# Kernel tuning notes

Measured on AMD Instinct MI355X. Metric: run time of the kernel, lower is better.

Reference implementation:

```python
import jax, jax.numpy as jnp
import numpy as np

D, H, K = 384, 6, 8

def _ln(x, g, b, eps=1e-5):
    mu = jnp.mean(x, axis=-1, keepdims=True)
    var = jnp.mean((x - mu) ** 2, axis=-1, keepdims=True)
    return (x - mu) * jax.lax.rsqrt(var + eps) * g + b

def setup_inputs() -> dict:
    key = jax.random.key(0)
    ks = jax.random.split(key, 20)
    B, N = 4, 2048
    s = 0.02
    inp = {
        'x': jax.random.normal(ks[0], (B, N, D), jnp.float32),
        'knn_index': jax.random.randint(ks[1], (B * K * N,), 0, B * N, jnp.int64),
        'ln1_g': jnp.ones((D,), jnp.float32),
        'ln1_b': jnp.zeros((D,), jnp.float32),
        'w_qkv': jax.random.normal(ks[2], (D, 3 * D), jnp.float32) * s,
        'w_proj': jax.random.normal(ks[3], (D, D), jnp.float32) * s,
        'b_proj': jnp.zeros((D,), jnp.float32),
        'w_knn': jax.random.normal(ks[4], (2 * D, D), jnp.float32) * s,
        'b_knn': jnp.zeros((D,), jnp.float32),
        'w_g1': jax.random.normal(ks[5], (2 * D, D), jnp.float32) * s,
        'b_g1': jnp.zeros((D,), jnp.float32),
        'w_g2': jax.random.normal(ks[6], (D, D), jnp.float32) * s,
        'b_g2': jnp.zeros((D,), jnp.float32),
        'ln2_g': jnp.ones((D,), jnp.float32),
        'ln2_b': jnp.zeros((D,), jnp.float32),
        'w_fc1': jax.random.normal(ks[7], (D, 4 * D), jnp.float32) * s,
        'b_fc1': jnp.zeros((4 * D,), jnp.float32),
        'w_fc2': jax.random.normal(ks[8], (4 * D, D), jnp.float32) * s,
        'b_fc2': jnp.zeros((D,), jnp.float32),
    }
    return inp

def reference(x, knn_index, ln1_g, ln1_b, w_qkv, w_proj, b_proj, w_knn, b_knn,
              w_g1, b_g1, w_g2, b_g2, ln2_g, ln2_b, w_fc1, b_fc1, w_fc2, b_fc2):
    B, N, _ = x.shape
    hd = D // H
    scale = hd ** -0.5
    nx = _ln(x, ln1_g, ln1_b)
    # --- self attention ---
    qkv = (nx @ w_qkv).reshape(B, N, 3, H, hd).transpose(2, 0, 3, 1, 4)  # [3,B,H,N,hd]
    q, k, v = qkv[0], qkv[1], qkv[2]
    attn = jax.nn.softmax(jnp.einsum('bhnd,bhmd->bhnm', q * scale, k), axis=-1)
    attn_out = jnp.einsum('bhnm,bhmd->bhnd', attn, v).transpose(0, 2, 1, 3).reshape(B, N, D)
    attn_out = attn_out @ w_proj + b_proj
    # --- EdgeConv-style graph feature: gather-concat-MLP-maxpool ---
    feat = nx.reshape(B * N, D)[knn_index].reshape(B, K, N, D)
    xe = jnp.broadcast_to(nx[:, None], (B, K, N, D))
    gf = jnp.concatenate([feat - xe, xe], axis=-1)  # [B,K,N,2D]
    knn_out = jnp.max(jax.nn.leaky_relu(gf @ w_knn + b_knn, 0.2), axis=1)  # [B,N,D]
    # --- salience gate ---
    gi = jnp.concatenate([attn_out, knn_out], axis=-1)
    gate = jax.nn.sigmoid(jax.nn.gelu(gi @ w_g1 + b_g1, approximate=False) @ w_g2 + b_g2)
    fused = (1 - gate) * attn_out + gate * knn_out
    x = x + fused
    # --- FFN ---
    h = jax.nn.gelu(_ln(x, ln2_g, ln2_b) @ w_fc1 + b_fc1, approximate=False)
    x = x + (h @ w_fc2 + b_fc2)
    return x
```

## Files before the change

kernel.cpp:

```cpp
#include <hip/hip_runtime.h>
#include <math.h>

typedef unsigned short u16;
typedef __attribute__((ext_vector_type(8))) short short8;
typedef __attribute__((ext_vector_type(4))) float floatx4;
typedef __attribute__((ext_vector_type(16))) float floatx16;
typedef __attribute__((ext_vector_type(4))) short sh4v;
typedef __attribute__((ext_vector_type(2))) unsigned uint2v;

union sh4u { sh4v v; u16 u[4]; };
union sh8u { short8 v; u16 u[8]; };
union sh8w { short8 v; unsigned w[4]; };

__device__ __forceinline__ floatx4 mfma16(short8 a, short8 b, floatx4 c) {
  return __builtin_amdgcn_mfma_f32_16x16x32_bf16(a, b, c, 0, 0, 0);
}
__device__ __forceinline__ floatx16 mfma32(short8 a, short8 b, floatx16 c) {
  return __builtin_amdgcn_mfma_f32_32x32x16_bf16(a, b, c, 0, 0, 0);
}

__device__ __forceinline__ floatx4 zero4() {
  floatx4 z = {0.f, 0.f, 0.f, 0.f};
  return z;
}
__device__ __forceinline__ floatx16 zero16() {
  floatx16 z;
#pragma unroll
  for (int i = 0; i < 16; i++) z[i] = 0.f;
  return z;
}

__device__ __forceinline__ float hexp2(float x) {
  return __builtin_amdgcn_exp2f(x);
}

__device__ __forceinline__ u16 f2b(float f) {
  union { float f; unsigned u; } v; v.f = f;
  unsigned u = v.u;
  return (u16)((u + 0x7FFFu + ((u >> 16) & 1u)) >> 16);
}

__device__ __forceinline__ float b2f(u16 u) {
  union { unsigned u; float f; } v; v.u = ((unsigned)u) << 16;
  return v.f;
}

__device__ __forceinline__ float blo(unsigned w) {
  union { unsigned u; float f; } v; v.u = w << 16;
  return v.f;
}
__device__ __forceinline__ float bhi(unsigned w) {
  union { unsigned u; float f; } v; v.u = w & 0xFFFF0000u;
  return v.f;
}

__device__ __forceinline__ float gelu_exact(float x) {
  return 0.5f * x * (1.f + erff(x * 0.70710678118654752440f));
}

__device__ __forceinline__ unsigned pack2(float a, float b) {
  return (unsigned)f2b(a) | ((unsigned)f2b(b) << 16);
}

__device__ __forceinline__ unsigned permpack(float p0, float p1) {
  return __builtin_amdgcn_perm(__float_as_uint(p1), __float_as_uint(p0), 0x07060302u);
}

__global__ __launch_bounds__(256) void tcln_kernel(
    const float* __restrict__ p0, const float* __restrict__ p1,
    const float* __restrict__ p2, const float* __restrict__ p3,
    const float* __restrict__ p4, const float* __restrict__ p5,
    const float* __restrict__ wknn,
    u16* __restrict__ o0, u16* __restrict__ o1, u16* __restrict__ o2,
    u16* __restrict__ o3, u16* __restrict__ o4, u16* __restrict__ o5,
    u16* __restrict__ wcT,
    const float* __restrict__ x, const float* __restrict__ g,
    const float* __restrict__ bia, u16* __restrict__ nx) {
  __shared__ u16 L[64][66];
  int t = blockIdx.x, tid = threadIdx.x;
  if (t >= 612) {
    int wave = tid >> 6, lane = tid & 63;
    int row = (t - 612) * 4 + wave;
    const float* xr = x + (size_t)row * 384;
    float v[6];
    float s = 0.f;
#pragma unroll
    for (int j = 0; j < 6; j++) { v[j] = xr[lane + 64 * j]; s += v[j]; }
#pragma unroll
    for (int off = 32; off > 0; off >>= 1) s += __shfl_xor(s, off);
    float mu = s * (1.f / 384.f);
    float ss = 0.f;
#pragma unroll
    for (int j = 0; j < 6; j++) { float d = v[j] - mu; ss += d * d; }
#pragma unroll
    for (int off = 32; off > 0; off >>= 1) ss += __shfl_xor(ss, off);
    float rstd = rsqrtf(ss * (1.f / 384.f) + 1e-5f);
    u16* orow = nx + (size_t)row * 384;
#pragma unroll
    for (int j = 0; j < 6; j++) {
      int d = lane + 64 * j;
      orow[d] = f2b((v[j] - mu) * rstd * g[d] + bia[d]);
    }
    return;
  }
  if (t >= 540) {
    t -= 540;
    int tk = t / 12, tn = t % 12;
    int k0 = tk * 64, j0 = tn * 64;
#pragma unroll
    for (int i = 0; i < 4; i++) {
      int c = tid + 256 * i;
      int r = c >> 4, c4 = (c & 15) * 4;
      floatx4 v;
      if (j0 < 384) {
        v = *(const floatx4*)(wknn + (size_t)(k0 + r) * 384 + j0 + c4);
      } else {
        floatx4 a = *(const floatx4*)(wknn + (size_t)(384 + k0 + r) * 384 + (j0 - 384) + c4);
        floatx4 b = *(const floatx4*)(wknn + (size_t)(k0 + r) * 384 + (j0 - 384) + c4);
        v = a - b;
      }
      *(unsigned*)&L[r][c4]     = pack2(v[0], v[1]);
      *(unsigned*)&L[r][c4 + 2] = pack2(v[2], v[3]);
    }
    __syncthreads();
#pragma unroll
    for (int i = 0; i < 2; i++) {
      int c = tid + 256 * i;
      int nn = c >> 3, k8 = (c & 7) * 8;
      sh8u pk;
#pragma unroll
      for (int j = 0; j < 8; j++) pk.u[j] = L[k8 + j][nn];
      *(short8*)(wcT + (size_t)(j0 + nn) * 384 + k0 + k8) = pk.v;
    }
    return;
  }
  const float* src; u16* dst; int Kd, Nd, tk, tn;
  if      (t < 108) { src = p0; dst = o0; Kd = 384;  Nd = 1152; tk = t / 18; tn = t % 18; }
  else if (t < 144) { src = p1; dst = o1; Kd = 384;  Nd = 384;  t -= 108; tk = t / 6;  tn = t % 6; }
  else if (t < 216) { src = p2; dst = o2; Kd = 768;  Nd = 384;  t -= 144; tk = t / 6;  tn = t % 6; }
  else if (t < 252) { src = p3; dst = o3; Kd = 384;  Nd = 384;  t -= 216; tk = t / 6;  tn = t % 6; }
  else if (t < 396) { src = p4; dst = o4; Kd = 384;  Nd = 1536; t -= 252; tk = t / 24; tn = t % 24; }
  else              { src = p5; dst = o5; Kd = 1536; Nd = 384;  t -= 396; tk = t / 6;  tn = t % 6; }
  int k0 = tk * 64, n0 = tn * 64;
#pragma unroll
  for (int i = 0; i < 4; i++) {
    int c = tid + 256 * i;
    int r = c >> 4, c4 = (c & 15) * 4;
    floatx4 v = *(const floatx4*)(src + (size_t)(k0 + r) * Nd + n0 + c4);
    *(unsigned*)&L[r][c4]     = pack2(v[0], v[1]);
    *(unsigned*)&L[r][c4 + 2] = pack2(v[2], v[3]);
  }
  __syncthreads();
#pragma unroll
  for (int i = 0; i < 2; i++) {
    int c = tid + 256 * i;
    int nn = c >> 3, k8 = (c & 7) * 8;
    sh8u pk;
#pragma unroll
    for (int j = 0; j < 8; j++) pk.u[j] = L[k8 + j][nn];
    *(short8*)(dst + (size_t)(n0 + nn) * Kd + k0 + k8) = pk.v;
  }
}

__global__ __launch_bounds__(256) void lnb_kernel(const u16* __restrict__ x,
                                                  const float* __restrict__ g,
                                                  const float* __restrict__ bia,
                                                  u16* __restrict__ out) {
  int wave = threadIdx.x >> 6, lane = threadIdx.x & 63;
  int row = blockIdx.x * 4 + wave;
  const u16* xr = x + (size_t)row * 384;
  float v[6];
  float s = 0.f;
#pragma unroll
  for (int j = 0; j < 6; j++) { v[j] = b2f(xr[lane + 64 * j]); s += v[j]; }
#pragma unroll
  for (int off = 32; off > 0; off >>= 1) s += __shfl_xor(s, off);
  float mu = s * (1.f / 384.f);
  float ss = 0.f;
#pragma unroll
  for (int j = 0; j < 6; j++) { float d = v[j] - mu; ss += d * d; }
#pragma unroll
  for (int off = 32; off > 0; off >>= 1) ss += __shfl_xor(ss, off);
  float rstd = rsqrtf(ss * (1.f / 384.f) + 1e-5f);
  u16* orow = out + (size_t)row * 384;
#pragma unroll
  for (int j = 0; j < 6; j++) {
    int d = lane + 64 * j;
    orow[d] = f2b((v[j] - mu) * rstd * g[d] + bia[d]);
  }
}

template <int EPI>
__global__ __launch_bounds__(256) void gemm64_kernel(
    const u16* __restrict__ A0, const u16* __restrict__ A1, int Ksplit,
    const u16* __restrict__ BwT, const u16* __restrict__ BwT2, int N, int K,
    const float* __restrict__ bias,
    float* __restrict__ outF, u16* __restrict__ outB, u16* __restrict__ outB2,
    const u16* __restrict__ eA16, const u16* __restrict__ eK16,
    const float* __restrict__ eX, u16* __restrict__ outV) {
  __shared__ u16 As[64][72];
  __shared__ u16 Bs[128][72];
  int tid = threadIdx.x;
  int lane = tid & 63, w = tid >> 6, quad = lane >> 4, l16 = lane & 15;
  int n0 = blockIdx.x * 128, m0 = blockIdx.y * 64;
  int ra = tid >> 3, ca = (tid & 7) * 8;
  const u16* Bsrc = BwT;
  int nbase = n0;
  if (EPI == 8 && n0 >= 1152) { Bsrc = BwT2; nbase = n0 - 1152; }
  floatx4 acc[4][2];
#pragma unroll
  for (int i = 0; i < 4; i++)
#pragma unroll
    for (int j = 0; j < 2; j++) acc[i][j] = zero4();

  short8 pa[2], pb[4];
  auto loadAB = [&](int k0) {
    const u16* Ap;
    int kk, sA;
    if (k0 < Ksplit) { Ap = A0; kk = k0; sA = Ksplit; }
    else             { Ap = A1; kk = k0 - Ksplit; sA = K - Ksplit; }
    pa[0] = *(const short8*)(Ap + (size_t)(m0 + ra) * sA + kk + ca);
    pa[1] = *(const short8*)(Ap + (size_t)(m0 + ra + 32) * sA + kk + ca);
#pragma unroll
    for (int i = 0; i < 4; i++)
      pb[i] = *(const short8*)(Bsrc + (size_t)(nbase + ra + 32 * i) * K + k0 + ca);
  };
  loadAB(0);
  int iters = K >> 6;
  for (int kt = 0; kt < iters; kt++) {
    __syncthreads();
    *(short8*)&As[ra][ca] = pa[0];
    *(short8*)&As[ra + 32][ca] = pa[1];
#pragma unroll
    for (int i = 0; i < 4; i++) *(short8*)&Bs[ra + 32 * i][ca] = pb[i];
    __syncthreads();
    if (kt + 1 < iters) loadAB((kt + 1) * 64);
#pragma unroll
    for (int kh = 0; kh < 2; kh++) {
      short8 af[4], bfr[2];
#pragma unroll
      for (int mt = 0; mt < 4; mt++)
        af[mt] = *(const short8*)&As[mt * 16 + l16][kh * 32 + quad * 8];
#pragma unroll
      for (int nt = 0; nt < 2; nt++)
        bfr[nt] = *(const short8*)&Bs[w * 32 + nt * 16 + l16][kh * 32 + quad * 8];
#pragma unroll
      for (int mt = 0; mt < 4; mt++)
#pragma unroll
        for (int nt = 0; nt < 2; nt++)
          acc[mt][nt] = mfma16(af[mt], bfr[nt], acc[mt][nt]);
    }
  }

#pragma unroll
  for (int mt = 0; mt < 4; mt++)
#pragma unroll
    for (int nt = 0; nt < 2; nt++) {
      int col = n0 + w * 32 + nt * 16 + l16;
      int row0 = m0 + mt * 16 + quad * 4;
      if (EPI == 8) {
        if (col < 1152) {
          float sc = (col < 384) ? 0.18033688011112042f : 1.f;
          sh4u pk;
#pragma unroll
          for (int r = 0; r < 4; r++) {
            u16 bv = f2b(acc[mt][nt][r] * sc);
            outB[(size_t)(row0 + r) * 1152 + col] = bv;
            pk.u[r] = bv;
          }
          if (col >= 768) {
            int b = row0 >> 11, n = row0 & 2047;
            int hd = col - 768;
            *(sh4v*)(outV + ((size_t)(b * 6 + (hd >> 6)) * 64 + (hd & 63)) * 2048 + n) = pk.v;
          }
        } else {
#pragma unroll
          for (int r = 0; r < 4; r++)
            outB2[(size_t)(row0 + r) * 768 + (col - 1152)] = f2b(acc[mt][nt][r]);
        }
      } else {
#pragma unroll
        for (int r = 0; r < 4; r++) {
          size_t rc = (size_t)(row0 + r) * N + col;
          float v = acc[mt][nt][r];
          if (EPI == 3) {
            outB[rc] = f2b(gelu_exact(v + bias[col]));
          } else if (EPI == 4) {
            float gte = 1.f / (1.f + hexp2(-1.44269504088896f * (v + bias[col])));
            float fu = (1.f - gte) * b2f(eA16[rc]) + gte * b2f(eK16[rc]);
            outB[rc] = f2b(eX[rc] + fu);
          } else if (EPI == 7) {
            outF[rc] = v + bias[col] + b2f(eA16[rc]);
          }
        }
      }
    }
}

__global__ __launch_bounds__(256) void attnknn_kernel(
    const u16* __restrict__ qkv, const u16* __restrict__ Vt,
    u16* __restrict__ OPb, float* __restrict__ LS,
    const u16* __restrict__ GBb, const int* __restrict__ kidx,
    const float* __restrict__ bknn, u16* __restrict__ knn_bf) {
  __shared__ u16 Ks[2][64][72];
  __shared__ u16 Vts[2][64][72];
  int bid = blockIdx.x, tid = threadIdx.x;
  int lane = tid & 63, w = tid >> 6;
  if (bid >= 1536) {
    int row = (bid - 1536) * 4 + w;
    int b = row >> 11, n = row & 2047;
    const unsigned* browp = (const unsigned*)(GBb + (size_t)row * 768 + 384);
    uint2v bw01 = *(const uint2v*)(browp + 2 * lane);
    unsigned bw2 = browp[128 + lane];
    floatx4 bk4 = *(const floatx4*)(bknn + 4 * lane);
    float bk40 = bknn[256 + 2 * lane], bk41 = bknn[256 + 2 * lane + 1];
    int gi[8];
#pragma unroll
    for (int kk = 0; kk < 8; kk++) gi[kk] = kidx[(b * 8 + kk) * 2048 + n];
    float mx[6];
#pragma unroll
    for (int e = 0; e < 6; e++) mx[e] = -1e30f;
#pragma unroll
    for (int kk = 0; kk < 8; kk++) {
      const unsigned* gp = (const unsigned*)(GBb + (size_t)gi[kk] * 768);
      uint2v g01 = *(const uint2v*)(gp + 2 * lane);
      unsigned g2 = gp[128 + lane];
      mx[0] = fmaxf(mx[0], blo(g01[0]));
      mx[1] = fmaxf(mx[1], bhi(g01[0]));
      mx[2] = fmaxf(mx[2], blo(g01[1]));
      mx[3] = fmaxf(mx[3], bhi(g01[1]));
      mx[4] = fmaxf(mx[4], blo(g2));
      mx[5] = fmaxf(mx[5], bhi(g2));
    }
    float vv[6];
    vv[0] = mx[0] + blo(bw01[0]) + bk4[0];
    vv[1] = mx[1] + bhi(bw01[0]) + bk4[1];
    vv[2] = mx[2] + blo(bw01[1]) + bk4[2];
    vv[3] = mx[3] + bhi(bw01[1]) + bk4[3];
    vv[4] = mx[4] + blo(bw2) + bk40;
    vv[5] = mx[5] + bhi(bw2) + bk41;
#pragma unroll
    for (int e = 0; e < 6; e++) vv[e] = fmaxf(vv[e], 0.2f * vv[e]);
    unsigned* op = (unsigned*)(knn_bf + (size_t)row * 384);
    uint2v ow;
    ow[0] = pack2(vv[0], vv[1]);
    ow[1] = pack2(vv[2], vv[3]);
    *(uint2v*)(op + 2 * lane) = ow;
    op[128 + lane] = pack2(vv[4], vv[5]);
    return;
  }
  int vb = (bid & 7) * 192 + (bid >> 3);
  int split = vb / 384;
  int rr = vb - split * 384;
  int bh = rr >> 4, b = bh / 6, h = bh % 6;
  int q0 = (rr & 15) * 128;
  int ql = lane & 31, h5 = lane >> 5;
  const u16* qbase = qkv + (size_t)b * 2048 * 1152 + h * 64;
  const u16* kbase = qbase + 384 + (size_t)split * 512 * 1152;
  const u16* vtb = Vt + (size_t)bh * 64 * 2048 + split * 512;
  int qrow = q0 + w * 32 + ql;
  short8 qB[4];
#pragma unroll
  for (int s = 0; s < 4; s++)
    qB[s] = *(const short8*)(qbase + (size_t)qrow * 1152 + s * 16 + h5 * 8);
  floatx16 O[2];
  O[0] = zero16(); O[1] = zero16();
  float accLs = 0.f;

  int rb = tid >> 3, c8 = (tid & 7) * 8;
  short8 rk[2], rv[2];
  rk[0] = *(const short8*)(kbase + (size_t)rb * 1152 + c8);
  rk[1] = *(const short8*)(kbase + (size_t)(rb + 32) * 1152 + c8);
  rv[0] = *(const short8*)(vtb + (size_t)rb * 2048 + c8);
  rv[1] = *(const short8*)(vtb + (size_t)(rb + 32) * 2048 + c8);

  int cur = 0;
  for (int kt = 0; kt < 8; kt++) {
    *(short8*)&Ks[cur][rb][c8] = rk[0];
    *(short8*)&Ks[cur][rb + 32][c8] = rk[1];
    *(short8*)&Vts[cur][rb][c8] = rv[0];
    *(short8*)&Vts[cur][rb + 32][c8] = rv[1];
    __syncthreads();
    if (kt < 7) {
      int key0 = (kt + 1) * 64;
      rk[0] = *(const short8*)(kbase + (size_t)(key0 + rb) * 1152 + c8);
      rk[1] = *(const short8*)(kbase + (size_t)(key0 + rb + 32) * 1152 + c8);
      rv[0] = *(const short8*)(vtb + (size_t)rb * 2048 + key0 + c8);
      rv[1] = *(const short8*)(vtb + (size_t)(rb + 32) * 2048 + key0 + c8);
    }
#pragma unroll
    for (int t = 0; t < 2; t++) {
      floatx16 st = zero16();
#pragma unroll
      for (int s = 0; s < 4; s++) {
        short8 aK = *(const short8*)&Ks[cur][32 * t + ql][16 * s + 8 * h5];
        st = mfma32(aK, qB[s], st);
      }
      unsigned W[8];
#pragma unroll
      for (int j = 0; j < 8; j++) {
        float e0 = hexp2(st[2 * j]), e1 = hexp2(st[2 * j + 1]);
        accLs += e0 + e1;
        W[j] = permpack(e0, e1);
      }
#pragma unroll
      for (int c = 0; c < 2; c++) {
        int kk = 2 * t + c;
        uint2v s0 = __builtin_amdgcn_permlane32_swap(W[4 * c], W[4 * c + 2], false, false);
        uint2v s1 = __builtin_amdgcn_permlane32_swap(W[4 * c + 1], W[4 * c + 3], false, false);
        sh8w pb_;
        pb_.w[0] = s0[0];
        pb_.w[1] = s1[0];
        pb_.w[2] = s0[1];
        pb_.w[3] = s1[1];
        short8 aV0 = *(const short8*)&Vts[cur][ql][16 * kk + 8 * h5];
        short8 aV1 = *(const short8*)&Vts[cur][32 + ql][16 * kk + 8 * h5];
        O[0] = mfma32(aV0, pb_.v, O[0]);
        O[1] = mfma32(aV1, pb_.v, O[1]);
      }
    }
    cur ^= 1;
  }
  u16* orow = OPb + (size_t)split * 8192 * 384 + (size_t)(b * 2048 + qrow) * 384 + h * 64;
#pragma unroll
  for (int d = 0; d < 2; d++)
#pragma unroll
    for (int rq = 0; rq < 4; rq++) {
      sh4u pk;
#pragma unroll
      for (int r3 = 0; r3 < 4; r3++) pk.u[r3] = f2b(O[d][4 * rq + r3]);
      *(sh4v*)(orow + 32 * d + 8 * rq + 4 * h5) = pk.v;
    }
  uint2v sw = __builtin_amdgcn_permlane32_swap(__float_as_uint(accLs), __float_as_uint(accLs),
                                               false, false);
  if (lane < 32) LS[split * 8192 + b * 2048 + qrow] = accLs + __uint_as_float(sw[1]);
}

__global__ __launch_bounds__(256) void projc_kernel(
    const u16* __restrict__ OPb, const float* __restrict__ LS,
    const u16* __restrict__ BwT, const float* __restrict__ bias,
    u16* __restrict__ outB) {
  __shared__ u16 As[64][72];
  __shared__ u16 Bs[128][72];
  int tid = threadIdx.x;
  int lane = tid & 63, w = tid >> 6, quad = lane >> 4, l16 = lane & 15;
  int n0 = blockIdx.x * 128, m0 = blockIdx.y * 64;
  int ra = tid >> 3, ca = (tid & 7) * 8;
  const size_t SP = (size_t)8192 * 384;
  floatx4 acc[4][2];
#pragma unroll
  for (int i = 0; i < 4; i++)
#pragma unroll
    for (int j = 0; j < 2; j++) acc[i][j] = zero4();

  short8 pa[2], pb[4];
  auto loadAB = [&](int k0) {
#pragma unroll
    for (int i = 0; i < 2; i++) {
      const u16* p = OPb + (size_t)(m0 + ra + 32 * i) * 384 + k0 + ca;
      sh8u a0, a1, a2, a3, pk;
      a0.v = *(const short8*)p;
      a1.v = *(const short8*)(p + SP);
      a2.v = *(const short8*)(p + 2 * SP);
      a3.v = *(const short8*)(p + 3 * SP);
#pragma unroll
      for (int j = 0; j < 8; j++)
        pk.u[j] = f2b((b2f(a0.u[j]) + b2f(a1.u[j])) + (b2f(a2.u[j]) + b2f(a3.u[j])));
      pa[i] = pk.v;
    }
#pragma unroll
    for (int i = 0; i < 4; i++)
      pb[i] = *(const short8*)(BwT + (size_t)(n0 + ra + 32 * i) * 384 + k0 + ca);
  };
  loadAB(0);
  for (int kt = 0; kt < 6; kt++) {
    __syncthreads();
    *(short8*)&As[ra][ca] = pa[0];
    *(short8*)&As[ra + 32][ca] = pa[1];
#pragma unroll
    for (int i = 0; i < 4; i++) *(short8*)&Bs[ra + 32 * i][ca] = pb[i];
    __syncthreads();
    if (kt < 5) loadAB((kt + 1) * 64);
#pragma unroll
    for (int kh = 0; kh < 2; kh++) {
      short8 af[4], bfr[2];
#pragma unroll
      for (int mt = 0; mt < 4; mt++)
        af[mt] = *(const short8*)&As[mt * 16 + l16][kh * 32 + quad * 8];
#pragma unroll
      for (int nt = 0; nt < 2; nt++)
        bfr[nt] = *(const short8*)&Bs[w * 32 + nt * 16 + l16][kh * 32 + quad * 8];
#pragma unroll
      for (int mt = 0; mt < 4; mt++)
#pragma unroll
        for (int nt = 0; nt < 2; nt++)
          acc[mt][nt] = mfma16(af[mt], bfr[nt], acc[mt][nt]);
    }
  }
#pragma unroll
  for (int mt = 0; mt < 4; mt++) {
    int row0 = m0 + mt * 16 + quad * 4;
    float rl[4];
#pragma unroll
    for (int r = 0; r < 4; r++) {
      int gr = row0 + r;
      rl[r] = 1.f / ((LS[gr] + LS[8192 + gr]) + (LS[16384 + gr] + LS[24576 + gr]));
    }
#pragma unroll
    for (int nt = 0; nt < 2; nt++) {
      int col = n0 + w * 32 + nt * 16 + l16;
#pragma unroll
      for (int r = 0; r < 4; r++)
        outB[(size_t)(row0 + r) * 384 + col] = f2b(acc[mt][nt][r] * rl[r] + bias[col]);
    }
  }
}

extern "C" void kernel_launch(void* const* d_in, const int* in_sizes, int n_in,
                              void* d_out, int out_size, void* d_ws, size_t ws_size,
                              hipStream_t stream) {
  const float* x    = (const float*)d_in[0];
  const int* kidx   = (const int*)d_in[1];
  const float* ln1g = (const float*)d_in[2];
  const float* ln1b = (const float*)d_in[3];
  const float* wqkv = (const float*)d_in[4];
  const float* wproj= (const float*)d_in[5];
  const float* bproj= (const float*)d_in[6];
  const float* wknn = (const float*)d_in[7];
  const float* bknn = (const float*)d_in[8];
  const float* wg1  = (const float*)d_in[9];
  const float* bg1  = (const float*)d_in[10];
  const float* wg2  = (const float*)d_in[11];
  const float* bg2  = (const float*)d_in[12];
  const float* ln2g = (const float*)d_in[13];
  const float* ln2b = (const float*)d_in[14];
  const float* wfc1 = (const float*)d_in[15];
  const float* bfc1 = (const float*)d_in[16];
  const float* wfc2 = (const float*)d_in[17];
  const float* bfc2 = (const float*)d_in[18];
  float* out = (float*)d_out;

  const int M = 8192;
  char* ws = (char*)d_ws;
  size_t off = 0;
  auto alloc = [&](size_t bytes) -> char* {
    char* p = ws + off;
    off += (bytes + 255) & ~(size_t)255;
    return p;
  };
  u16* nx_bf    = (u16*)alloc((size_t)M * 384 * 2);
  u16* qkv_bf   = (u16*)alloc((size_t)M * 1152 * 2);
  u16* attn_bf  = (u16*)alloc((size_t)M * 384 * 2);
  u16* GBb      = (u16*)alloc((size_t)M * 768 * 2);
  u16* knn_bf   = (u16*)alloc((size_t)M * 384 * 2);
  u16* x2b      = (u16*)alloc((size_t)M * 384 * 2);
  u16* t1_bf    = (u16*)alloc((size_t)M * 384 * 2);
  u16* nx2_bf   = (u16*)alloc((size_t)M * 384 * 2);
  u16* Vt_b     = (u16*)alloc((size_t)24 * 64 * 2048 * 2);
  u16* OPb      = (u16*)alloc((size_t)4 * M * 384 * 2);
  float* LS     = (float*)alloc((size_t)4 * M * 4);
  u16* wqkvT    = (u16*)alloc((size_t)1152 * 384 * 2);
  u16* wprojT   = (u16*)alloc(384 * 384 * 2);
  u16* wcT      = (u16*)alloc((size_t)768 * 384 * 2);
  u16* wg1T     = (u16*)alloc((size_t)384 * 768 * 2);
  u16* wg2T     = (u16*)alloc(384 * 384 * 2);
  u16* wfc1T    = (u16*)alloc((size_t)1536 * 384 * 2);
  u16* wfc2T    = (u16*)alloc((size_t)384 * 1536 * 2);
  u16* h_bf     = qkv_bf;

  tcln_kernel<<<2660, 256, 0, stream>>>(wqkv, wproj, wg1, wg2, wfc1, wfc2, wknn,
                                        wqkvT, wprojT, wg1T, wg2T, wfc1T, wfc2T, wcT,
                                        x, ln1g, ln1b, nx_bf);
  gemm64_kernel<8><<<dim3(15, 128), 256, 0, stream>>>(nx_bf, nx_bf, 384, wqkvT, wcT, 1920, 384,
                                                      nullptr, nullptr, qkv_bf, GBb,
                                                      nullptr, nullptr, nullptr, Vt_b);
  attnknn_kernel<<<3584, 256, 0, stream>>>(qkv_bf, Vt_b, OPb, LS,
                                           GBb, kidx, bknn, knn_bf);
  projc_kernel<<<dim3(3, 128), 256, 0, stream>>>(OPb, LS, wprojT, bproj, attn_bf);
  gemm64_kernel<3><<<dim3(3, 128), 256, 0, stream>>>(attn_bf, knn_bf, 384, wg1T, nullptr, 384, 768,
                                                     bg1, nullptr, t1_bf, nullptr,
                                                     nullptr, nullptr, nullptr, nullptr);
  gemm64_kernel<4><<<dim3(3, 128), 256, 0, stream>>>(t1_bf, t1_bf, 384, wg2T, nullptr, 384, 384,
                                                     bg2, nullptr, x2b, nullptr,
                                                     attn_bf, knn_bf, x, nullptr);
  lnb_kernel<<<2048, 256, 0, stream>>>(x2b, ln2g, ln2b, nx2_bf);
  gemm64_kernel<3><<<dim3(12, 128), 256, 0, stream>>>(nx2_bf, nx2_bf, 384, wfc1T, nullptr, 1536, 384,
                                                      bfc1, nullptr, h_bf, nullptr,
                                                      nullptr, nullptr, nullptr, nullptr);
  gemm64_kernel<7><<<dim3(3, 128), 256, 0, stream>>>(h_bf, h_bf, 1536, wfc2T, nullptr, 384, 1536,
                                                     bfc2, out, nullptr, nullptr,
                                                     x2b, nullptr, nullptr, nullptr);
  (void)in_sizes; (void)n_in; (void)out_size; (void)ws_size;
}
```

Measured before the change: 261.3 us.

## Stage GEMM tiles with direct global-to-LDS loads and XOR-swizzled shared layout

The shared GEMM kernel now uses global_load_lds to copy A and B tiles straight into LDS instead of going through registers and then storing to shared memory. The padded shared arrays are replaced by unpadded ones with an XOR swizzle on the k-column to avoid bank conflicts. The next tile is issued after the compute and a barrier, so there is only a single buffer and less overlap of load with compute. A template parameter for the M tile size is added but every launch uses 64.

```diff
diff --git a/kernel.cpp b/kernel.cpp
--- a/kernel.cpp
+++ b/kernel.cpp
@@ -64,6 +64,12 @@
 
 __device__ __forceinline__ unsigned permpack(float p0, float p1) {
   return __builtin_amdgcn_perm(__float_as_uint(p1), __float_as_uint(p0), 0x07060302u);
+}
+
+__device__ __forceinline__ void gload16(const u16* g, u16* l) {
+  __builtin_amdgcn_global_load_lds(
+      (const __attribute__((address_space(1))) unsigned*)(const void*)g,
+      (__attribute__((address_space(3))) unsigned*)(void*)l, 16, 0, 0);
 }
 
 __global__ __launch_bounds__(256) void tcln_kernel(
@@ -190,7 +196,7 @@
   }
 }
 
-template <int EPI>
+template <int EPI, int MR>
 __global__ __launch_bounds__(256) void gemm64_kernel(
     const u16* __restrict__ A0, const u16* __restrict__ A1, int Ksplit,
     const u16* __restrict__ BwT, const u16* __restrict__ BwT2, int N, int K,
@@ -198,62 +204,68 @@
     float* __restrict__ outF, u16* __restrict__ outB, u16* __restrict__ outB2,
     const u16* __restrict__ eA16, const u16* __restrict__ eK16,
     const float* __restrict__ eX, u16* __restrict__ outV) {
-  __shared__ u16 As[64][72];
-  __shared__ u16 Bs[128][72];
+  const int MT = MR / 16;
+  __shared__ u16 As[MR][64];
+  __shared__ u16 Bs[128][64];
   int tid = threadIdx.x;
   int lane = tid & 63, w = tid >> 6, quad = lane >> 4, l16 = lane & 15;
-  int n0 = blockIdx.x * 128, m0 = blockIdx.y * 64;
-  int ra = tid >> 3, ca = (tid & 7) * 8;
+  int n0 = blockIdx.x * 128, m0 = blockIdx.y * MR;
   const u16* Bsrc = BwT;
   int nbase = n0;
   if (EPI == 8 && n0 >= 1152) { Bsrc = BwT2; nbase = n0 - 1152; }
-  floatx4 acc[4][2];
-#pragma unroll
-  for (int i = 0; i < 4; i++)
+  floatx4 acc[MT][2];
+#pragma unroll
+  for (int i = 0; i < MT; i++)
 #pragma unroll
     for (int j = 0; j < 2; j++) acc[i][j] = zero4();
 
-  short8 pa[2], pb[4];
-  auto loadAB = [&](int k0) {
+  int r8 = lane >> 3, s8 = lane & 7;
+  int ksw = (s8 ^ r8) * 8;
+  auto stage = [&](int k0) {
     const u16* Ap;
     int kk, sA;
     if (k0 < Ksplit) { Ap = A0; kk = k0; sA = Ksplit; }
     else             { Ap = A1; kk = k0 - Ksplit; sA = K - Ksplit; }
-    pa[0] = *(const short8*)(Ap + (size_t)(m0 + ra) * sA + kk + ca);
-    pa[1] = *(const short8*)(Ap + (size_t)(m0 + ra + 32) * sA + kk + ca);
-#pragma unroll
-    for (int i = 0; i < 4; i++)
-      pb[i] = *(const short8*)(Bsrc + (size_t)(nbase + ra + 32 * i) * K + k0 + ca);
+#pragma unroll
+    for (int p = 0; p < MR / 32; p++) {
+      int rw = p * 32 + w * 8;
+      gload16(Ap + (size_t)(m0 + rw + r8) * sA + kk + ksw, &As[rw][0]);
+    }
+#pragma unroll
+    for (int p = 0; p < 4; p++) {
+      int rw = p * 32 + w * 8;
+      gload16(Bsrc + (size_t)(nbase + rw + r8) * K + k0 + ksw, &Bs[rw][0]);
+    }
   };
-  loadAB(0);
+  stage(0);
+  int x7 = l16 & 7;
+  int co0 = (quad ^ x7) * 8;
+  int co1 = ((quad + 4) ^ x7) * 8;
   int iters = K >> 6;
   for (int kt = 0; kt < iters; kt++) {
     __syncthreads();
-    *(short8*)&As[ra][ca] = pa[0];
-    *(short8*)&As[ra + 32][ca] = pa[1];
-#pragma unroll
-    for (int i = 0; i < 4; i++) *(short8*)&Bs[ra + 32 * i][ca] = pb[i];
-    __syncthreads();
-    if (kt + 1 < iters) loadAB((kt + 1) * 64);
 #pragma unroll
     for (int kh = 0; kh < 2; kh++) {
-      short8 af[4], bfr[2];
-#pragma unroll
-      for (int mt = 0; mt < 4; mt++)
-        af[mt] = *(const short8*)&As[mt * 16 + l16][kh * 32 + quad * 8];
+      int co = kh ? co1 : co0;
+      short8 af[MT], bfr[2];
+#pragma unroll
+      for (int mt = 0; mt < MT; mt++)
+        af[mt] = *(const short8*)&As[mt * 16 + l16][co];
 #pragma unroll
       for (int nt = 0; nt < 2; nt++)
-        bfr[nt] = *(const short8*)&Bs[w * 32 + nt * 16 + l16][kh * 32 + quad * 8];
-#pragma unroll
-      for (int mt = 0; mt < 4; mt++)
+        bfr[nt] = *(const short8*)&Bs[w * 32 + nt * 16 + l16][co];
+#pragma unroll
+      for (int mt = 0; mt < MT; mt++)
 #pragma unroll
         for (int nt = 0; nt < 2; nt++)
           acc[mt][nt] = mfma16(af[mt], bfr[nt], acc[mt][nt]);
     }
-  }
-
-#pragma unroll
-  for (int mt = 0; mt < 4; mt++)
+    __syncthreads();
+    if (kt + 1 < iters) stage((kt + 1) * 64);
+  }
+
+#pragma unroll
+  for (int mt = 0; mt < MT; mt++)
 #pragma unroll
     for (int nt = 0; nt < 2; nt++) {
       int col = n0 + w * 32 + nt * 16 + l16;
@@ -571,24 +583,24 @@
   tcln_kernel<<<2660, 256, 0, stream>>>(wqkv, wproj, wg1, wg2, wfc1, wfc2, wknn,
                                         wqkvT, wprojT, wg1T, wg2T, wfc1T, wfc2T, wcT,
                                         x, ln1g, ln1b, nx_bf);
-  gemm64_kernel<8><<<dim3(15, 128), 256, 0, stream>>>(nx_bf, nx_bf, 384, wqkvT, wcT, 1920, 384,
-                                                      nullptr, nullptr, qkv_bf, GBb,
-                                                      nullptr, nullptr, nullptr, Vt_b);
+  gemm64_kernel<8, 64><<<dim3(15, 128), 256, 0, stream>>>(nx_bf, nx_bf, 384, wqkvT, wcT, 1920, 384,
+                                                          nullptr, nullptr, qkv_bf, GBb,
+                                                          nullptr, nullptr, nullptr, Vt_b);
   attnknn_kernel<<<3584, 256, 0, stream>>>(qkv_bf, Vt_b, OPb, LS,
                                            GBb, kidx, bknn, knn_bf);
   projc_kernel<<<dim3(3, 128), 256, 0, stream>>>(OPb, LS, wprojT, bproj, attn_bf);
-  gemm64_kernel<3><<<dim3(3, 128), 256, 0, stream>>>(attn_bf, knn_bf, 384, wg1T, nullptr, 384, 768,
-                                                     bg1, nullptr, t1_bf, nullptr,
-                                                     nullptr, nullptr, nullptr, nullptr);
-  gemm64_kernel<4><<<dim3(3, 128), 256, 0, stream>>>(t1_bf, t1_bf, 384, wg2T, nullptr, 384, 384,
-                                                     bg2, nullptr, x2b, nullptr,
-                                                     attn_bf, knn_bf, x, nullptr);
+  gemm64_kernel<3, 64><<<dim3(3, 128), 256, 0, stream>>>(attn_bf, knn_bf, 384, wg1T, nullptr, 384, 768,
+                                                         bg1, nullptr, t1_bf, nullptr,
+                                                         nullptr, nullptr, nullptr, nullptr);
+  gemm64_kernel<4, 64><<<dim3(3, 128), 256, 0, stream>>>(t1_bf, t1_bf, 384, wg2T, nullptr, 384, 384,
+                                                         bg2, nullptr, x2b, nullptr,
+                                                         attn_bf, knn_bf, x, nullptr);
   lnb_kernel<<<2048, 256, 0, stream>>>(x2b, ln2g, ln2b, nx2_bf);
-  gemm64_kernel<3><<<dim3(12, 128), 256, 0, stream>>>(nx2_bf, nx2_bf, 384, wfc1T, nullptr, 1536, 384,
-                                                      bfc1, nullptr, h_bf, nullptr,
-                                                      nullptr, nullptr, nullptr, nullptr);
-  gemm64_kernel<7><<<dim3(3, 128), 256, 0, stream>>>(h_bf, h_bf, 1536, wfc2T, nullptr, 384, 1536,
-                                                     bfc2, out, nullptr, nullptr,
-                                                     x2b, nullptr, nullptr, nullptr);
+  gemm64_kernel<3, 64><<<dim3(12, 128), 256, 0, stream>>>(nx2_bf, nx2_bf, 384, wfc1T, nullptr, 1536, 384,
+                                                          bfc1, nullptr, h_bf, nullptr,
+                                                          nullptr, nullptr, nullptr, nullptr);
+  gemm64_kernel<7, 64><<<dim3(3, 128), 256, 0, stream>>>(h_bf, h_bf, 1536, wfc2T, nullptr, 384, 1536,
+                                                         bfc2, out, nullptr, nullptr,
+                                                         x2b, nullptr, nullptr, nullptr);
   (void)in_sizes; (void)n_in; (void)out_size; (void)ws_size;
 }
```

Result: slower. 277.1 us (+6.1%).
